# Performance work log

Measured on AMD Instinct MI355X. Metric: run time of the kernel, lower is better.

## Reference

```python
import jax, jax.numpy as jnp
import numpy as np
import itertools

N = 600000
CIN = 64
COUT = 64
KS = 3
STRIDE = 2
DIL = 1
GRID = 256        # coordinate range before striding
M = 512           # per-axis key radix (fits int32 keys for batch<=2)
SHIFT = (KS - 1) // 2 * DIL   # keeps shifted coords non-negative under neighbor offsets
SENT = 2 ** 30    # sentinel key for padded unique slots
BN_EPS = 1e-5

OFFSETS = list(itertools.product(range(-(KS // 2), KS // 2 + 1), repeat=3))  # 27 offsets, row-major


def setup_inputs() -> dict:
    key = jax.random.key(0)
    k1, k2, k3, k4, k5, k6, k7, k8 = jax.random.split(key, 8)
    xyz = jax.random.randint(k1, (N, 3), 0, GRID, dtype=jnp.int32)
    b = jax.random.randint(k2, (N, 1), 0, 2, dtype=jnp.int32)  # batch of 2 scenes
    coords = jnp.concatenate([xyz, b], axis=1)                 # [N,4] = (x,y,z,batch)
    feats = jax.random.normal(k3, (N, CIN), dtype=jnp.float32)
    weight = jax.random.normal(k4, (27, CIN, COUT), dtype=jnp.float32) / np.sqrt(27 * CIN)
    bn_scale = jax.random.uniform(k5, (COUT,), jnp.float32, 0.5, 1.5)
    bn_bias = jax.random.normal(k6, (COUT,), jnp.float32) * 0.1
    bn_mean = jax.random.normal(k7, (COUT,), jnp.float32) * 0.1
    bn_var = jax.random.uniform(k8, (COUT,), jnp.float32, 0.5, 1.5)
    return {"coords": coords, "feats": feats, "weight": weight,
            "bn_scale": bn_scale, "bn_bias": bn_bias, "bn_mean": bn_mean, "bn_var": bn_var}


def _encode(xyz, b):
    # pack (batch, x, y, z) into a single sortable int32 key
    return ((b * M + xyz[:, 0] + SHIFT) * M + (xyz[:, 1] + SHIFT)) * M + (xyz[:, 2] + SHIFT)


def _forward(coords, feats, weight, bn_scale, bn_bias, bn_mean, bn_var):
    # --- stride path: voxel downsample via unique + scatter-add (index_add) ---
    xyz = coords[:, :3] // STRIDE
    b = coords[:, 3]
    keys = _encode(xyz, b)                                   # [N]
    ukeys, inv = jnp.unique(keys, size=N, fill_value=SENT, return_inverse=True)  # sorted, padded
    fds = jax.ops.segment_sum(feats, inv, num_segments=N)    # pooled feats [N, CIN]
    valid = ukeys < SENT                                      # real (non-padded) voxels

    # --- sparse 3x3x3 conv at stride 1 (output coords == input coords) ---
    # gather(neighbor) -> matmul(W_k) -> accumulate, per kernel offset
    out = jnp.zeros((N, COUT), dtype=feats.dtype)
    for k, (dx, dy, dz) in enumerate(OFFSETS):
        delta = ((dx * M) + dy) * M + dz
        q = ukeys + delta * DIL
        pos = jnp.clip(jnp.searchsorted(ukeys, q), 0, N - 1)
        match = (ukeys[pos] == q) & valid
        gathered = jnp.where(match[:, None], fds[pos], 0.0)   # [N, CIN]
        out = out + gathered @ weight[k]

    # --- BatchNorm (eval-mode running stats) + ReLU ---
    inv_std = jax.lax.rsqrt(bn_var + BN_EPS)
    out = (out - bn_mean) * (bn_scale * inv_std) + bn_bias
    out = jax.nn.relu(out)
    return jnp.where(valid[:, None], out, 0.0)                # zero padded rows


def reference(coords, feats, weight, bn_scale, bn_bias, bn_mean, bn_var):
    return _forward(coords, feats, weight, bn_scale, bn_bias, bn_mean, bn_var)
```

## Files before the change

### kernel.cpp

```cpp
#include <hip/hip_runtime.h>
#include <hip/hip_bf16.h>

#define NPTS 600000
#define NKEYS (1 << 22)
#define CHUNK 4096
#define NPART (NKEYS / CHUNK)

typedef unsigned int u32;
typedef unsigned short u16;
typedef __attribute__((ext_vector_type(8))) short short8;
typedef __attribute__((ext_vector_type(4))) float f32x4;

__device__ __forceinline__ u16 f2bf(float x) {
  union { float f; u32 u; } c; c.f = x;
  u32 r = c.u + 0x7fffu + ((c.u >> 16) & 1u);
  return (u16)(r >> 16);
}

__global__ void k0a_bn(const float* __restrict__ s, const float* __restrict__ b,
                       const float* __restrict__ m, const float* __restrict__ v,
                       float* __restrict__ ab) {
  int c = threadIdx.x;
  float a = s[c] * rsqrtf(v[c] + 1e-5f);
  ab[c] = a;
  ab[64 + c] = b[c] - m[c] * a;
}

__global__ void k0b_wt(const float* __restrict__ W, u16* __restrict__ Wt) {
  int e = blockIdx.x * 256 + threadIdx.x;
  if (e >= 27 * 4096) return;
  int k = e >> 12, rem = e & 4095, cin = rem >> 6, cout = rem & 63;
  Wt[(k << 12) + (cout << 6) + cin] = f2bf(W[e]);
}

__global__ void k1_keys(const int* __restrict__ coords, int* __restrict__ keys,
                        u32* __restrict__ lut) {
  int i = blockIdx.x * 256 + threadIdx.x;
  if (i >= NPTS) return;
  int4 c4 = *(const int4*)(coords + i * 4);
  int k = (c4.w << 21) | ((c4.x >> 1) << 14) | ((c4.y >> 1) << 7) | (c4.z >> 1);
  keys[i] = k;
  atomicAdd(&lut[k], 1u);
}

__global__ void k2a_part(const u32* __restrict__ lut, u32* __restrict__ partials) {
  __shared__ u32 sd[256];
  int blk = blockIdx.x, t = threadIdx.x;
  const u32* p = lut + blk * CHUNK;
  u32 s = 0;
  for (int j = t; j < CHUNK; j += 256) s += (p[j] != 0u);
  sd[t] = s; __syncthreads();
  for (int o = 128; o > 0; o >>= 1) { if (t < o) sd[t] += sd[t + o]; __syncthreads(); }
  if (t == 0) partials[blk] = sd[0];
}

__global__ void k2b_top(u32* __restrict__ partials) {
  __shared__ u32 sh[NPART];
  int t = threadIdx.x;
  u32 x = partials[t];
  sh[t] = x; __syncthreads();
  for (int off = 1; off < NPART; off <<= 1) {
    u32 add = (t >= off) ? sh[t - off] : 0u;
    __syncthreads();
    sh[t] += add;
    __syncthreads();
  }
  partials[t] = sh[t] - x;
  if (t == NPART - 1) partials[NPART] = sh[t];
}

__global__ void k2c_fill(u32* __restrict__ lut, const u32* __restrict__ partials,
                         int* __restrict__ r2k, float* __restrict__ fds32) {
  __shared__ u32 tsum[256];
  int blk = blockIdx.x, t = threadIdx.x;
  int base = blk * CHUNK + t * 16;
  u32 loc[16]; u32 s = 0;
#pragma unroll
  for (int j = 0; j < 16; j++) { loc[j] = lut[base + j]; s += (loc[j] != 0u); }
  tsum[t] = s; __syncthreads();
  for (int off = 1; off < 256; off <<= 1) {
    u32 add = (t >= off) ? tsum[t - off] : 0u;
    __syncthreads();
    tsum[t] += add;
    __syncthreads();
  }
  u32 rank = partials[blk] + tsum[t] - s;
#pragma unroll
  for (int j = 0; j < 16; j++) {
    if (loc[j]) {
      u32 flag = (loc[j] > 1u) ? 0x80000000u : 0u;
      lut[base + j] = (rank + 1u) | flag;
      r2k[rank] = base + j;
      if (flag) {
        float4 z = {0.f, 0.f, 0.f, 0.f};
        float* d = fds32 + ((size_t)rank << 6);
#pragma unroll
        for (int c = 0; c < 16; c++) *(float4*)(d + c * 4) = z;
      }
      rank++;
    } else lut[base + j] = 0u;
  }
}

__global__ void k3_seg(const float* __restrict__ feats, const int* __restrict__ keys,
                       const u32* __restrict__ lut, float* __restrict__ fds32,
                       u16* __restrict__ fdsb) {
  int idx = blockIdx.x * 256 + threadIdx.x;
  if (idx >= NPTS * 16) return;
  int i = idx >> 4, q = (idx & 15) << 2;
  u32 lv = lut[keys[i]];
  u32 r = (lv & 0x7fffffffu) - 1u;
  float4 v = *(const float4*)(feats + (size_t)i * 64 + q);
  if (lv >> 31) {
    float* dst = fds32 + ((size_t)r << 6) + q;
    atomicAdd(dst + 0, v.x); atomicAdd(dst + 1, v.y);
    atomicAdd(dst + 2, v.z); atomicAdd(dst + 3, v.w);
  } else {
    ushort4 o;
    o.x = f2bf(v.x); o.y = f2bf(v.y); o.z = f2bf(v.z); o.w = f2bf(v.w);
    *(ushort4*)(fdsb + ((size_t)r << 6) + q) = o;
  }
}

__global__ void k3b_fix(const int* __restrict__ r2k, const u32* __restrict__ lut,
                        const u32* __restrict__ pU,
                        const float* __restrict__ fds32, u16* __restrict__ fdsb) {
  int idx = blockIdx.x * 256 + threadIdx.x;
  int r = idx >> 2;
  if (r >= (int)(*pU)) return;
  u32 lv = lut[r2k[r]];
  if (!(lv >> 31)) return;
  int q = (idx & 3) << 4;
  const float* src = fds32 + ((size_t)r << 6) + q;
  u16* dst = fdsb + ((size_t)r << 6) + q;
#pragma unroll
  for (int j = 0; j < 4; j++) {
    float4 v = *(const float4*)(src + j * 4);
    ushort4 o;
    o.x = f2bf(v.x); o.y = f2bf(v.y); o.z = f2bf(v.z); o.w = f2bf(v.w);
    *(ushort4*)(dst + j * 4) = o;
  }
}

__global__ __launch_bounds__(320) void k4_conv(
    const u32* __restrict__ lut, const int* __restrict__ r2k,
    const u16* __restrict__ fdsb, const u16* __restrict__ Wt,
    const u32* __restrict__ pU, const float* __restrict__ ab,
    float* __restrict__ out) {
  __shared__ __align__(16) char ldsA[5][8192];
  const u32 U = *pU;
  int tid = threadIdx.x;
  int w = tid >> 6, l = tid & 63;
  int bid = blockIdx.x;
  int cpx = (int)gridDim.x >> 3;
  int swz = (bid & 7) * cpx + (bid >> 3);
  int rbase = swz * 64;

  int key = -1, x = 0, y = 0, z = 0;
  if (w == 0) {
    int r = rbase + l;
    key = ((u32)r < U) ? r2k[r] : -1;
    z = key & 127; y = (key >> 7) & 127; x = (key >> 14) & 127;
  }
  u32 lvr[4];

#define PROBE(T) { \
    const int dx_ = (T) / 9 - 1, dy_ = ((T) / 3) % 3 - 1, dz_ = (T) % 3 - 1; \
    int nx_ = x + dx_, ny_ = y + dy_, nz_ = z + dz_; \
    bool ok_ = (key >= 0) & ((u32)nx_ < 128u) & ((u32)ny_ < 128u) & ((u32)nz_ < 128u); \
    int a_ = ok_ ? (key + dx_ * 16384 + dy_ * 128 + dz_) : NKEYS; \
    lvr[(T) & 3] = lut[a_]; }

#define GLD(T) { \
    u32 lv_ = lvr[(T) & 3]; \
    u32 row_ = lv_ ? ((lv_ & 0x7fffffffu) - 1u) : (u32)NPTS; \
    const char* fr_ = (const char*)(fdsb + ((size_t)row_ << 6)); \
    char* sl_ = &ldsA[(T) % 5][0]; \
    __builtin_amdgcn_global_load_lds((const __attribute__((address_space(1))) void*)(fr_ +   0), (__attribute__((address_space(3))) void*)(sl_ +    0), 16, 0, 0); \
    __builtin_amdgcn_global_load_lds((const __attribute__((address_space(1))) void*)(fr_ +  16), (__attribute__((address_space(3))) void*)(sl_ + 1024), 16, 0, 0); \
    __builtin_amdgcn_global_load_lds((const __attribute__((address_space(1))) void*)(fr_ +  32), (__attribute__((address_space(3))) void*)(sl_ + 2048), 16, 0, 0); \
    __builtin_amdgcn_global_load_lds((const __attribute__((address_space(1))) void*)(fr_ +  48), (__attribute__((address_space(3))) void*)(sl_ + 3072), 16, 0, 0); \
    __builtin_amdgcn_global_load_lds((const __attribute__((address_space(1))) void*)(fr_ +  64), (__attribute__((address_space(3))) void*)(sl_ + 4096), 16, 0, 0); \
    __builtin_amdgcn_global_load_lds((const __attribute__((address_space(1))) void*)(fr_ +  80), (__attribute__((address_space(3))) void*)(sl_ + 5120), 16, 0, 0); \
    __builtin_amdgcn_global_load_lds((const __attribute__((address_space(1))) void*)(fr_ +  96), (__attribute__((address_space(3))) void*)(sl_ + 6144), 16, 0, 0); \
    __builtin_amdgcn_global_load_lds((const __attribute__((address_space(1))) void*)(fr_ + 112), (__attribute__((address_space(3))) void*)(sl_ + 7168), 16, 0, 0); }

  int ct = w - 1;
  int col = l & 15, kg = l >> 4;
  f32x4 acc[4] = {};

#define CONSUME(K) { \
    const char* sl_ = &ldsA[(K) % 5][0]; \
    const u16* wk_ = Wt + ((K) << 12) + (((ct << 4) + col) << 6) + (kg << 3); \
    short8 b0_ = *(const short8*)(wk_); \
    short8 b1_ = *(const short8*)(wk_ + 32); \
    short8 a0_[4], a1_[4]; \
    _Pragma("unroll") for (int rt = 0; rt < 4; rt++) { \
      int row_ = (rt << 4) + col; \
      a0_[rt] = *(const short8*)(sl_ + (kg << 10) + (row_ << 4)); \
      a1_[rt] = *(const short8*)(sl_ + ((kg + 4) << 10) + (row_ << 4)); } \
    _Pragma("unroll") for (int rt = 0; rt < 4; rt++) { \
      acc[rt] = __builtin_amdgcn_mfma_f32_16x16x32_bf16(a0_[rt], b0_, acc[rt], 0, 0, 0); \
      acc[rt] = __builtin_amdgcn_mfma_f32_16x16x32_bf16(a1_[rt], b1_, acc[rt], 0, 0, 0); } }

#define NWAIT(K) ( (((K)-1) < 24 ? 8 : 0) + (((K)-1) < 21 ? 1 : 0) + \
                   (((K)     < 24) ? 8 : 0) + (((K)     < 21) ? 1 : 0) )

#define BODY(K) { \
    if (w == 0) { \
      if ((K) + 3 < 27) GLD((K) + 3) \
      if ((K) + 6 < 27) PROBE((K) + 6) \
      asm volatile("s_waitcnt vmcnt(%0)" :: "n"(NWAIT(K)) : "memory"); \
    } else { \
      CONSUME(K) \
    } \
    asm volatile("" ::: "memory"); \
    __builtin_amdgcn_s_barrier(); \
    asm volatile("" ::: "memory"); }

  if (w == 0) {
    PROBE(0) PROBE(1) PROBE(2) PROBE(3)
    asm volatile("s_waitcnt vmcnt(0)" ::: "memory");
    GLD(0)
    asm volatile("s_waitcnt vmcnt(0)" ::: "memory");
    PROBE(4) GLD(1) PROBE(5) GLD(2)
  }
  asm volatile("" ::: "memory");
  __builtin_amdgcn_s_barrier();
  asm volatile("" ::: "memory");

  BODY(0)  BODY(1)  BODY(2)  BODY(3)  BODY(4)  BODY(5)  BODY(6)
  BODY(7)  BODY(8)  BODY(9)  BODY(10) BODY(11) BODY(12) BODY(13)
  BODY(14) BODY(15) BODY(16) BODY(17) BODY(18) BODY(19) BODY(20)
  BODY(21) BODY(22) BODY(23) BODY(24) BODY(25) BODY(26)

#undef PROBE
#undef GLD
#undef CONSUME
#undef NWAIT
#undef BODY

  if (w > 0) {
    int c = (ct << 4) | col;
    float al = ab[c], be = ab[64 + c];
#pragma unroll
    for (int rt = 0; rt < 4; rt++) {
#pragma unroll
      for (int i = 0; i < 4; i++) {
        int r = rbase + (rt << 4) + (kg << 2) + i;
        if (r >= NPTS) continue;
        bool valid = ((u32)r < U);
        float vv = 0.f;
        if (valid) {
          vv = fmaf(acc[rt][i], al, be);
          vv = vv > 0.f ? vv : 0.f;
        }
        out[((size_t)r << 6) + c] = vv;
      }
    }
  }
}

extern "C" void kernel_launch(void* const* d_in, const int* in_sizes, int n_in,
                              void* d_out, int out_size, void* d_ws, size_t ws_size,
                              hipStream_t stream) {
  const int*   coords = (const int*)d_in[0];
  const float* feats  = (const float*)d_in[1];
  const float* W      = (const float*)d_in[2];
  const float* bns    = (const float*)d_in[3];
  const float* bnb    = (const float*)d_in[4];
  const float* bnm    = (const float*)d_in[5];
  const float* bnv    = (const float*)d_in[6];
  float* out = (float*)d_out;

  char* ws = (char*)d_ws;
  size_t off = 0;
  auto alloc = [&](size_t bytes) -> void* {
    void* p = ws + off;
    off += (bytes + 255) & ~(size_t)255;
    return p;
  };
  u32* lut      = (u32*)alloc((size_t)(NKEYS + 1) * 4);
  u32* partials = (u32*)alloc((NPART + 8) * 4);
  int* keys     = (int*)alloc((size_t)NPTS * 4);
  int* r2k      = (int*)alloc((size_t)NPTS * 4);
  u16* fdsb     = (u16*)alloc((size_t)(NPTS + 1) * 64 * 2);
  u16* Wt       = (u16*)alloc((size_t)27 * 4096 * 2);
  float* ab     = (float*)alloc(128 * 4);
  (void)ws_size; (void)out_size; (void)n_in; (void)in_sizes;

  float* fds32 = out;

  hipMemsetAsync(lut, 0, (size_t)(NKEYS + 1) * 4, stream);
  hipMemsetAsync(fdsb + (size_t)NPTS * 64, 0, 128, stream);

  k0a_bn<<<1, 64, 0, stream>>>(bns, bnb, bnm, bnv, ab);
  k0b_wt<<<(27 * 4096 + 255) / 256, 256, 0, stream>>>(W, Wt);
  k1_keys<<<(NPTS + 255) / 256, 256, 0, stream>>>(coords, keys, lut);
  k2a_part<<<NPART, 256, 0, stream>>>(lut, partials);
  k2b_top<<<1, NPART, 0, stream>>>(partials);
  k2c_fill<<<NPART, 256, 0, stream>>>(lut, partials, r2k, fds32);
  k3_seg<<<(NPTS * 16 + 255) / 256, 256, 0, stream>>>(feats, keys, lut, fds32, fdsb);
  k3b_fix<<<(NPTS * 4 + 255) / 256, 256, 0, stream>>>(r2k, lut, partials + NPART, fds32, fdsb);
  k4_conv<<<(NPTS + 63) / 64, 320, 0, stream>>>(lut, r2k, fdsb, Wt,
                                                partials + NPART, ab, out);
}
```

Before: 557.1 us.

## Stage conv neighbor rows through registers with swizzled LDS and grouped barriers

The producer wave in the sparse conv kernel no longer uses direct global-to-LDS loads. It now loads each neighbor feature row into registers, with missing neighbors zeroed so the padding row and its memset go away, and writes them to LDS with a per-row rotation swizzle to avoid bank conflicts. The pipeline is regrouped into super-steps of three kernel offsets per barrier with six LDS slots, which cuts the barrier count from 27 to 9. The trade-off is higher register pressure in the producer wave and an extra register-to-LDS pass, in exchange for fewer synchronisations and conflict-free MFMA operand reads.

Result: slower. 637.3 us (+14.4%).

```diff
diff --git a/kernel.cpp b/kernel.cpp
--- a/kernel.cpp
+++ b/kernel.cpp
@@ -147,7 +147,7 @@
     const u16* __restrict__ fdsb, const u16* __restrict__ Wt,
     const u32* __restrict__ pU, const float* __restrict__ ab,
     float* __restrict__ out) {
-  __shared__ __align__(16) char ldsA[5][8192];
+  __shared__ __align__(16) char ldsA[6][8192];
   const u32 U = *pU;
   int tid = threadIdx.x;
   int w = tid >> 6, l = tid & 63;
@@ -162,83 +162,84 @@
     key = ((u32)r < U) ? r2k[r] : -1;
     z = key & 127; y = (key >> 7) & 127; x = (key >> 14) & 127;
   }
-  u32 lvr[4];
+  u32 lvr[6];
+  short8 rg[3][8];
+  const short8 z8 = {0, 0, 0, 0, 0, 0, 0, 0};
 
 #define PROBE(T) { \
     const int dx_ = (T) / 9 - 1, dy_ = ((T) / 3) % 3 - 1, dz_ = (T) % 3 - 1; \
     int nx_ = x + dx_, ny_ = y + dy_, nz_ = z + dz_; \
     bool ok_ = (key >= 0) & ((u32)nx_ < 128u) & ((u32)ny_ < 128u) & ((u32)nz_ < 128u); \
     int a_ = ok_ ? (key + dx_ * 16384 + dy_ * 128 + dz_) : NKEYS; \
-    lvr[(T) & 3] = lut[a_]; }
-
-#define GLD(T) { \
-    u32 lv_ = lvr[(T) & 3]; \
-    u32 row_ = lv_ ? ((lv_ & 0x7fffffffu) - 1u) : (u32)NPTS; \
-    const char* fr_ = (const char*)(fdsb + ((size_t)row_ << 6)); \
-    char* sl_ = &ldsA[(T) % 5][0]; \
-    __builtin_amdgcn_global_load_lds((const __attribute__((address_space(1))) void*)(fr_ +   0), (__attribute__((address_space(3))) void*)(sl_ +    0), 16, 0, 0); \
-    __builtin_amdgcn_global_load_lds((const __attribute__((address_space(1))) void*)(fr_ +  16), (__attribute__((address_space(3))) void*)(sl_ + 1024), 16, 0, 0); \
-    __builtin_amdgcn_global_load_lds((const __attribute__((address_space(1))) void*)(fr_ +  32), (__attribute__((address_space(3))) void*)(sl_ + 2048), 16, 0, 0); \
-    __builtin_amdgcn_global_load_lds((const __attribute__((address_space(1))) void*)(fr_ +  48), (__attribute__((address_space(3))) void*)(sl_ + 3072), 16, 0, 0); \
-    __builtin_amdgcn_global_load_lds((const __attribute__((address_space(1))) void*)(fr_ +  64), (__attribute__((address_space(3))) void*)(sl_ + 4096), 16, 0, 0); \
-    __builtin_amdgcn_global_load_lds((const __attribute__((address_space(1))) void*)(fr_ +  80), (__attribute__((address_space(3))) void*)(sl_ + 5120), 16, 0, 0); \
-    __builtin_amdgcn_global_load_lds((const __attribute__((address_space(1))) void*)(fr_ +  96), (__attribute__((address_space(3))) void*)(sl_ + 6144), 16, 0, 0); \
-    __builtin_amdgcn_global_load_lds((const __attribute__((address_space(1))) void*)(fr_ + 112), (__attribute__((address_space(3))) void*)(sl_ + 7168), 16, 0, 0); }
+    lvr[(T) % 6] = lut[a_]; }
+
+#define LOADRG(T) { \
+    u32 lv_ = lvr[(T) % 6]; \
+    _Pragma("unroll") for (int j = 0; j < 8; j++) rg[(T) % 3][j] = z8; \
+    if (lv_) { \
+      const u16* fr_ = fdsb + ((size_t)((lv_ & 0x7fffffffu) - 1u) << 6); \
+      _Pragma("unroll") for (int j = 0; j < 8; j++) \
+        rg[(T) % 3][j] = *(const short8*)(fr_ + j * 8); } }
+
+#define DSW(T) { \
+    char* dst_ = &ldsA[(T) % 6][l * 128]; \
+    int r7_ = l & 7; \
+    _Pragma("unroll") for (int j = 0; j < 8; j++) \
+      *(short8*)(dst_ + (((j + r7_) & 7) << 4)) = rg[(T) % 3][j]; }
 
   int ct = w - 1;
   int col = l & 15, kg = l >> 4;
   f32x4 acc[4] = {};
 
 #define CONSUME(K) { \
-    const char* sl_ = &ldsA[(K) % 5][0]; \
     const u16* wk_ = Wt + ((K) << 12) + (((ct << 4) + col) << 6) + (kg << 3); \
     short8 b0_ = *(const short8*)(wk_); \
     short8 b1_ = *(const short8*)(wk_ + 32); \
-    short8 a0_[4], a1_[4]; \
+    const char* slab_ = &ldsA[(K) % 6][0]; \
     _Pragma("unroll") for (int rt = 0; rt < 4; rt++) { \
       int row_ = (rt << 4) + col; \
-      a0_[rt] = *(const short8*)(sl_ + (kg << 10) + (row_ << 4)); \
-      a1_[rt] = *(const short8*)(sl_ + ((kg + 4) << 10) + (row_ << 4)); } \
-    _Pragma("unroll") for (int rt = 0; rt < 4; rt++) { \
-      acc[rt] = __builtin_amdgcn_mfma_f32_16x16x32_bf16(a0_[rt], b0_, acc[rt], 0, 0, 0); \
-      acc[rt] = __builtin_amdgcn_mfma_f32_16x16x32_bf16(a1_[rt], b1_, acc[rt], 0, 0, 0); } }
-
-#define NWAIT(K) ( (((K)-1) < 24 ? 8 : 0) + (((K)-1) < 21 ? 1 : 0) + \
-                   (((K)     < 24) ? 8 : 0) + (((K)     < 21) ? 1 : 0) )
-
-#define BODY(K) { \
-    if (w == 0) { \
-      if ((K) + 3 < 27) GLD((K) + 3) \
-      if ((K) + 6 < 27) PROBE((K) + 6) \
-      asm volatile("s_waitcnt vmcnt(%0)" :: "n"(NWAIT(K)) : "memory"); \
-    } else { \
-      CONSUME(K) \
-    } \
+      const char* rp_ = slab_ + row_ * 128; \
+      int r7_ = row_ & 7; \
+      short8 a0_ = *(const short8*)(rp_ + (((kg + r7_) & 7) << 4)); \
+      short8 a1_ = *(const short8*)(rp_ + (((kg + 4 + r7_) & 7) << 4)); \
+      acc[rt] = __builtin_amdgcn_mfma_f32_16x16x32_bf16(a0_, b0_, acc[rt], 0, 0, 0); \
+      acc[rt] = __builtin_amdgcn_mfma_f32_16x16x32_bf16(a1_, b1_, acc[rt], 0, 0, 0); } }
+
+#define BAR() { \
     asm volatile("" ::: "memory"); \
+    asm volatile("s_waitcnt lgkmcnt(0)" ::: "memory"); \
     __builtin_amdgcn_s_barrier(); \
     asm volatile("" ::: "memory"); }
 
   if (w == 0) {
-    PROBE(0) PROBE(1) PROBE(2) PROBE(3)
-    asm volatile("s_waitcnt vmcnt(0)" ::: "memory");
-    GLD(0)
-    asm volatile("s_waitcnt vmcnt(0)" ::: "memory");
-    PROBE(4) GLD(1) PROBE(5) GLD(2)
-  }
-  asm volatile("" ::: "memory");
-  __builtin_amdgcn_s_barrier();
-  asm volatile("" ::: "memory");
-
-  BODY(0)  BODY(1)  BODY(2)  BODY(3)  BODY(4)  BODY(5)  BODY(6)
-  BODY(7)  BODY(8)  BODY(9)  BODY(10) BODY(11) BODY(12) BODY(13)
-  BODY(14) BODY(15) BODY(16) BODY(17) BODY(18) BODY(19) BODY(20)
-  BODY(21) BODY(22) BODY(23) BODY(24) BODY(25) BODY(26)
+    PROBE(0) PROBE(1) PROBE(2) PROBE(3) PROBE(4) PROBE(5)
+    LOADRG(0) LOADRG(1) LOADRG(2)
+    DSW(0) DSW(1) DSW(2)
+    PROBE(6) PROBE(7) PROBE(8)
+    LOADRG(3) LOADRG(4) LOADRG(5)
+    PROBE(9) PROBE(10) PROBE(11)
+  }
+  BAR()
+
+#define SUPER(S) { \
+    if (w == 0) { \
+      if (3*(S)+3  < 27) DSW(3*(S)+3)  if (3*(S)+4  < 27) DSW(3*(S)+4)  if (3*(S)+5  < 27) DSW(3*(S)+5) \
+      if (3*(S)+6  < 27) LOADRG(3*(S)+6)  if (3*(S)+7  < 27) LOADRG(3*(S)+7)  if (3*(S)+8  < 27) LOADRG(3*(S)+8) \
+      if (3*(S)+9  < 27) PROBE(3*(S)+9)   if (3*(S)+10 < 27) PROBE(3*(S)+10)  if (3*(S)+11 < 27) PROBE(3*(S)+11) \
+    } else { \
+      CONSUME(3*(S)) CONSUME(3*(S)+1) CONSUME(3*(S)+2) \
+    } \
+    BAR() }
+
+  SUPER(0) SUPER(1) SUPER(2) SUPER(3) SUPER(4)
+  SUPER(5) SUPER(6) SUPER(7) SUPER(8)
 
 #undef PROBE
-#undef GLD
+#undef LOADRG
+#undef DSW
 #undef CONSUME
-#undef NWAIT
-#undef BODY
+#undef BAR
+#undef SUPER
 
   if (w > 0) {
     int c = (ct << 4) | col;
@@ -292,7 +293,6 @@
   float* fds32 = out;
 
   hipMemsetAsync(lut, 0, (size_t)(NKEYS + 1) * 4, stream);
-  hipMemsetAsync(fdsb + (size_t)NPTS * 64, 0, 128, stream);
 
   k0a_bn<<<1, 64, 0, stream>>>(bns, bnb, bnm, bnv, ab);
   k0b_wt<<<(27 * 4096 + 255) / 256, 256, 0, stream>>>(W, Wt);
```
